# Kernel tuning notes

Hardware: AMD Instinct MI355X
Metric: run time of the kernel (lower is better)

The kernel has to match this reference:

```python
import jax, jax.numpy as jnp
import numpy as np
import itertools
from jax import lax

B, CIN, COUT, RES, NH = 32, 512, 512, 56, 8
STRIDE = RES // 7  # 8 -> post-stride grid is 7x7 (N=49)
HD = COUT // NH    # 64


def _affine(x, s, b):  # BatchNorm2d in inference form (per-channel scale/shift)
    return x * s[None, :, None, None] + b[None, :, None, None]


def _conv1x1(x, w):  # w: [O, C]
    return jnp.einsum('oc,bchw->bohw', w, x)


def _conv3x3(x, w, stride, groups):
    return lax.conv_general_dilated(
        x, w, window_strides=(stride, stride), padding=[(1, 1), (1, 1)],
        feature_group_count=groups, dimension_numbers=('NCHW', 'OIHW', 'NCHW'))


def _bias_idx():
    points = list(itertools.product(range(7), range(7)))
    offsets, idxs = {}, []
    for p1 in points:
        for p2 in points:
            off = (abs(p1[0] - p2[0]), abs(p1[1] - p2[1]))
            if off not in offsets:
                offsets[off] = len(offsets)
            idxs.append(offsets[off])
    return np.array(idxs, dtype=np.int32).reshape(49, 49), len(offsets)


def setup_inputs() -> dict:
    key = jax.random.key(0)
    ks = jax.random.split(key, 24)
    idx_np, n_off = _bias_idx()  # n_off = 49
    rn = lambda k, sh, sc: jax.random.normal(k, sh, dtype=jnp.float32) * sc
    return {
        'x': rn(ks[0], (B, CIN, RES, RES), 1.0),
        'dw_w': rn(ks[1], (CIN, 1, 3, 3), 0.2),
        'bn0_s': 1.0 + rn(ks[2], (CIN,), 0.05), 'bn0_b': rn(ks[3], (CIN,), 0.05),
        'wq': rn(ks[4], (COUT, CIN), 0.03),
        'bnq_s': 1.0 + rn(ks[5], (COUT,), 0.05), 'bnq_b': rn(ks[6], (COUT,), 0.05),
        'wk': rn(ks[7], (COUT, CIN), 0.03),
        'bnk_s': 1.0 + rn(ks[8], (COUT,), 0.05), 'bnk_b': rn(ks[9], (COUT,), 0.05),
        'wv': rn(ks[10], (COUT, CIN), 0.03),
        'bnv_s': 1.0 + rn(ks[11], (COUT,), 0.05), 'bnv_b': rn(ks[12], (COUT,), 0.05),
        'loc_w': rn(ks[13], (COUT, COUT // NH, 3, 3), 0.05), 'loc_b': rn(ks[14], (COUT,), 0.02),
        'bnl_s': 1.0 + rn(ks[15], (COUT,), 0.05), 'bnl_b': rn(ks[16], (COUT,), 0.05),
        'th1': rn(ks[17], (NH, NH), 0.3), 'th2': rn(ks[18], (NH, NH), 0.3),
        'logit_scale': jnp.log(10.0) * jnp.ones((NH, 1, 1), dtype=jnp.float32),
        'ab': rn(ks[19], (NH, n_off), 0.02),
        'wo': rn(ks[20], (COUT, COUT), 0.03),
        'bno_s': 1.0 + rn(ks[21], (COUT,), 0.05), 'bno_b': rn(ks[22], (COUT,), 0.05),
        'bias_idx': jnp.array(idx_np),
    }


def reference(x, dw_w, bn0_s, bn0_b, wq, bnq_s, bnq_b, wk, bnk_s, bnk_b,
              wv, bnv_s, bnv_b, loc_w, loc_b, bnl_s, bnl_b, th1, th2,
              logit_scale, ab, wo, bno_s, bno_b, bias_idx):
    # stride_conv: depthwise 3x3 stride-8 + BN -> [B, C, 7, 7]
    x = _affine(_conv3x3(x, dw_w, STRIDE, CIN), bn0_s, bn0_b)
    Bc, C, H, W = x.shape
    N = H * W  # 49
    q = _affine(_conv1x1(x, wq), bnq_s, bnq_b).reshape(Bc, NH, HD, N).transpose(0, 1, 3, 2)  # [B,H,N,d]
    k = _affine(_conv1x1(x, wk), bnk_s, bnk_b).reshape(Bc, NH, HD, N)                        # [B,H,d,N]
    v4 = _affine(_conv1x1(x, wv), bnv_s, bnv_b)                                              # [B,Cout,7,7]
    v_local = _affine(_conv3x3(v4, loc_w, 1, NH) + loc_b[None, :, None, None], bnl_s, bnl_b)
    v = v4.reshape(Bc, NH, HD, N).transpose(0, 1, 3, 2)                                      # [B,H,N,d]
    # faithful to source: q normalized over head_dim, k normalized over token axis (last)
    qn = q / jnp.maximum(jnp.linalg.norm(q, axis=-1, keepdims=True), 1e-12)
    kn = k / jnp.maximum(jnp.linalg.norm(k, axis=-1, keepdims=True), 1e-12)
    ls = jnp.exp(jnp.minimum(logit_scale, jnp.log(100.0)))  # clamp max then exp
    attn = jnp.einsum('bhnd,bhdm->bhnm', qn, kn) * ls + ab[:, bias_idx]  # [B,H,49,49]
    attn = jnp.einsum('ij,bjnm->binm', th1, attn)   # talking head 1
    attn = jax.nn.softmax(attn, axis=-1)
    attn = jnp.einsum('ij,bjnm->binm', th2, attn)   # talking head 2
    out = jnp.einsum('bhnm,bhmd->bhnd', attn, v)    # [B,H,N,d]
    out = out.transpose(0, 1, 3, 2).reshape(Bc, COUT, H, W) + v_local
    out = jax.image.resize(out, (Bc, COUT, H * STRIDE, W * STRIDE), method='bilinear')
    out = out * jax.nn.relu6(out + 3.0) / 6.0       # Hardswish
    return _affine(_conv1x1(out, wo), bno_s, bno_b)
```

## Files before the change

### kernel.cpp

```cpp
#include <hip/hip_runtime.h>
#include <hip/hip_bf16.h>
#include <stdint.h>

typedef short short8 __attribute__((ext_vector_type(8)));
typedef float f32x4 __attribute__((ext_vector_type(4)));

#define NB    32
#define NC    512
#define NHD   8
#define HDD   64
#define N7    49
#define RES   56
#define P56   3136
#define NTOK  1568
#define NTOKP 1664
#define NBIG  100352
#define KDIM  512
#define KLOC  576

__device__ __forceinline__ void gload_lds16(const __hip_bfloat16* g, __hip_bfloat16* l) {
  __builtin_amdgcn_global_load_lds(
      (const __attribute__((address_space(1))) void*)g,
      (__attribute__((address_space(3))) void*)l, 16, 0, 0);
}

__global__ __launch_bounds__(256) void k_cvt(
    const float* __restrict__ s0, const float* __restrict__ s1,
    const float* __restrict__ s2, const float* __restrict__ s3,
    const float* __restrict__ s4,
    __hip_bfloat16* __restrict__ d0, __hip_bfloat16* __restrict__ d1,
    __hip_bfloat16* __restrict__ d2, __hip_bfloat16* __restrict__ d3,
    __hip_bfloat16* __restrict__ d4) {
  const float* s; __hip_bfloat16* d; int n = NC * NC;
  switch (blockIdx.y) {
    case 0: s = s0; d = d0; break;
    case 1: s = s1; d = d1; break;
    case 2: s = s2; d = d2; break;
    case 3: s = s3; d = d3; break;
    default: s = s4; d = d4; n = NC * KLOC; break;
  }
  for (int i = blockIdx.x * blockDim.x + threadIdx.x; i < n; i += gridDim.x * blockDim.x)
    d[i] = __float2bfloat16(s[i]);
}

__global__ __launch_bounds__(64) void k_stride(
    const float* __restrict__ x, const float* __restrict__ dw,
    const float* __restrict__ s0, const float* __restrict__ b0,
    __hip_bfloat16* __restrict__ xs) {
  const int ci = blockIdx.x, b = blockIdx.y, t = threadIdx.x;
  __shared__ float rows[21][56];
  const float* xp = x + ((size_t)(b * NC + ci)) * RES * RES;
  for (int r = t; r < 21 * 56; r += 64) {
    int rr = r / 56, cc = r - rr * 56;
    int oh = rr / 3, kh = rr - oh * 3;
    int ih = oh * 8 + kh - 1;
    rows[rr][cc] = (ih >= 0) ? xp[ih * 56 + cc] : 0.f;
  }
  float w[9];
#pragma unroll
  for (int j = 0; j < 9; ++j) w[j] = dw[ci * 9 + j];
  const float sc = s0[ci], bi = b0[ci];
  __syncthreads();
  if (t < 49) {
    const int oh = t / 7, ow = t - oh * 7;
    float acc = 0.f;
#pragma unroll
    for (int kh = 0; kh < 3; ++kh)
#pragma unroll
      for (int kw = 0; kw < 3; ++kw) {
        int col = ow * 8 + kw - 1;
        float v = (col >= 0) ? rows[oh * 3 + kh][col] : 0.f;
        acc += v * w[kh * 3 + kw];
      }
    xs[(size_t)(b * 49 + t) * NC + ci] = __float2bfloat16(acc * sc + bi);
  }
}

__global__ __launch_bounds__(512) void k_gemm_big(
    const __hip_bfloat16* __restrict__ A,
    const __hip_bfloat16* __restrict__ Bm,
    const float* __restrict__ scale, const float* __restrict__ bias,
    float* __restrict__ out) {
  __shared__ __align__(16) __hip_bfloat16 lds[2][2][256 * 64];
  const int t = threadIdx.x;
  const int cpx = gridDim.x >> 3;
  const int nid = (blockIdx.x & 7) * cpx + (blockIdx.x >> 3);
  const int m0 = (nid & 1) * 256, n0 = (nid >> 1) * 256;

  const int lane = t & 63, wid = t >> 6;
  const int wm = (wid >> 2) * 128, wn = (wid & 3) * 64;
  const int fr = lane & 15, fq = lane >> 4;
  const int sw = fr & 7;

  const int srow = t >> 3;
  const int scol = ((t & 7) ^ ((t >> 3) & 7)) * 8;
  const __hip_bfloat16* Ab = A  + (size_t)(m0 + srow) * KDIM + scol;
  const __hip_bfloat16* Bb = Bm + (size_t)(n0 + srow) * KDIM + scol;

  const f32x4 fz = {0.f, 0.f, 0.f, 0.f};
  f32x4 acc[8][4];
#pragma unroll
  for (int i = 0; i < 8; ++i)
#pragma unroll
    for (int j = 0; j < 4; ++j) acc[i][j] = fz;

#define STAGE_BIG(d, kt)                                                      \
  do {                                                                        \
    const int kofs = (kt) * 64;                                               \
    gload_lds16(Ab + kofs,              &lds[d][0][wid * 512]);               \
    gload_lds16(Ab + kofs +  64 * KDIM, &lds[d][0][4096  + wid * 512]);       \
    gload_lds16(Ab + kofs + 128 * KDIM, &lds[d][0][8192  + wid * 512]);       \
    gload_lds16(Ab + kofs + 192 * KDIM, &lds[d][0][12288 + wid * 512]);       \
    gload_lds16(Bb + kofs,              &lds[d][1][wid * 512]);               \
    gload_lds16(Bb + kofs +  64 * KDIM, &lds[d][1][4096  + wid * 512]);       \
    gload_lds16(Bb + kofs + 128 * KDIM, &lds[d][1][8192  + wid * 512]);       \
    gload_lds16(Bb + kofs + 192 * KDIM, &lds[d][1][12288 + wid * 512]);       \
  } while (0)

  STAGE_BIG(0, 0);
  STAGE_BIG(1, 1);
  int cur = 0;
#pragma unroll 1
  for (int it = 0; it < 8; ++it) {
    if (it < 7) asm volatile("s_waitcnt vmcnt(8)" ::: "memory");
    else        asm volatile("s_waitcnt vmcnt(0)" ::: "memory");
    __builtin_amdgcn_sched_barrier(0);
    __builtin_amdgcn_s_barrier();
    __builtin_amdgcn_sched_barrier(0);
    const __hip_bfloat16* lap = lds[cur][0];
    const __hip_bfloat16* lbp = lds[cur][1];
#pragma unroll
    for (int ks = 0; ks < 2; ++ks) {
      short8 af[8], bf[4];
      const int c16 = ((ks * 4 + fq) ^ sw) * 8;
#pragma unroll
      for (int mi = 0; mi < 8; ++mi)
        af[mi] = *(const short8*)(lap + (wm + mi * 16 + fr) * 64 + c16);
#pragma unroll
      for (int ni = 0; ni < 4; ++ni)
        bf[ni] = *(const short8*)(lbp + (wn + ni * 16 + fr) * 64 + c16);
      __builtin_amdgcn_s_setprio(1);
#pragma unroll
      for (int mi = 0; mi < 8; ++mi)
#pragma unroll
        for (int ni = 0; ni < 4; ++ni)
          acc[mi][ni] = __builtin_amdgcn_mfma_f32_16x16x32_bf16(af[mi], bf[ni], acc[mi][ni], 0, 0, 0);
      __builtin_amdgcn_s_setprio(0);
    }
    __builtin_amdgcn_sched_barrier(0);
    __builtin_amdgcn_s_barrier();
    __builtin_amdgcn_sched_barrier(0);
    if (it < 6) STAGE_BIG(cur, it + 2);
    cur ^= 1;
  }
#undef STAGE_BIG

#pragma unroll
  for (int mi = 0; mi < 8; ++mi) {
#pragma unroll
    for (int ni = 0; ni < 4; ++ni) {
      const int gn = n0 + wn + ni * 16 + fr;
      const int outer = gn / P56;
      const int ii = gn - outer * P56;
#pragma unroll
      for (int r = 0; r < 4; ++r) {
        const int co = m0 + wm + mi * 16 + fq * 4 + r;
        out[((size_t)outer * NC + co) * P56 + ii] = acc[mi][ni][r] * scale[co] + bias[co];
      }
    }
  }
}

__global__ __launch_bounds__(256) void k_gemm_qkv(
    const __hip_bfloat16* __restrict__ wqb, const __hip_bfloat16* __restrict__ wkb,
    const __hip_bfloat16* __restrict__ wvb, const __hip_bfloat16* __restrict__ xs,
    const float* __restrict__ sq, const float* __restrict__ bq,
    const float* __restrict__ sk, const float* __restrict__ bk,
    const float* __restrict__ sv, const float* __restrict__ bv,
    float* __restrict__ qb, float* __restrict__ kb, float* __restrict__ vb) {
  __shared__ __align__(16) __hip_bfloat16 la[2][128 * 32];
  __shared__ __align__(16) __hip_bfloat16 lb[2][128 * 32];
  const int t = threadIdx.x;
  const int nwg = gridDim.x;
  const int orig = blockIdx.x;
  const int q = nwg >> 3, r = nwg & 7;
  const int xcd = orig & 7, pos = orig >> 3;
  const int nid = (xcd < r ? xcd * (q + 1) : r * (q + 1) + (xcd - r) * q) + pos;
  const int mt = nid % 12, nt = nid / 12;
  const int n0 = nt * 128, m0 = (mt & 3) * 128, sel = mt >> 2;

  const __hip_bfloat16* A = (sel == 0 ? wqb : sel == 1 ? wkb : wvb);
  const float* scale = (sel == 0 ? sq : sel == 1 ? sk : sv);
  const float* bias  = (sel == 0 ? bq : sel == 1 ? bk : bv);
  float* out = (sel == 0 ? qb : sel == 1 ? kb : vb);

  const int lane = t & 63, wid = t >> 6;
  const int wm = (wid >> 1) * 64, wn = (wid & 1) * 64;
  const int fr = lane & 15, fq = lane >> 4, kg = fq * 8;
  const int rA0 = wid * 16;
  const int grow = lane >> 2;
  const int gcol = (lane & 3) * 8;

  const f32x4 fz = {0.f, 0.f, 0.f, 0.f};
  f32x4 acc[4][4];
#pragma unroll
  for (int i = 0; i < 4; ++i)
#pragma unroll
    for (int j = 0; j < 4; ++j) acc[i][j] = fz;

  const __hip_bfloat16* Ab = A + (size_t)(m0 + rA0 + grow) * KDIM + gcol;
  const __hip_bfloat16* Bb = xs + (size_t)(n0 + rA0 + grow) * KDIM + gcol;

#define STAGE_QKV(buf, k0)                                        \
  do {                                                            \
    gload_lds16(Ab + (k0),             la[buf] + rA0 * 32);       \
    gload_lds16(Ab + (k0) + 64 * KDIM, la[buf] + (rA0 + 64) * 32);\
    gload_lds16(Bb + (k0),             lb[buf] + rA0 * 32);       \
    gload_lds16(Bb + (k0) + 64 * KDIM, lb[buf] + (rA0 + 64) * 32);\
  } while (0)

  STAGE_QKV(0, 0);
  STAGE_QKV(1, 32);
  int cur = 0;
#pragma unroll 1
  for (int it = 0; it < 16; ++it) {
    if (it < 15) asm volatile("s_waitcnt vmcnt(4)" ::: "memory");
    else         asm volatile("s_waitcnt vmcnt(0)" ::: "memory");
    __builtin_amdgcn_sched_barrier(0);
    __builtin_amdgcn_s_barrier();
    __builtin_amdgcn_sched_barrier(0);
    const __hip_bfloat16* lap = la[cur];
    const __hip_bfloat16* lbp = lb[cur];
    short8 af[4], bf[4];
#pragma unroll
    for (int mi = 0; mi < 4; ++mi) af[mi] = *(const short8*)(lap + (wm + mi * 16 + fr) * 32 + kg);
#pragma unroll
    for (int ni = 0; ni < 4; ++ni) bf[ni] = *(const short8*)(lbp + (wn + ni * 16 + fr) * 32 + kg);
#pragma unroll
    for (int mi = 0; mi < 4; ++mi)
#pragma unroll
      for (int ni = 0; ni < 4; ++ni)
        acc[mi][ni] = __builtin_amdgcn_mfma_f32_16x16x32_bf16(af[mi], bf[ni], acc[mi][ni], 0, 0, 0);
    __builtin_amdgcn_sched_barrier(0);
    __builtin_amdgcn_s_barrier();
    __builtin_amdgcn_sched_barrier(0);
    if (it < 14) STAGE_QKV(cur, (it + 2) * 32);
    cur ^= 1;
  }
#undef STAGE_QKV

#pragma unroll
  for (int mi = 0; mi < 4; ++mi) {
#pragma unroll
    for (int ni = 0; ni < 4; ++ni) {
      const int gn = n0 + wn + ni * 16 + fr;
      if (gn >= NTOK) continue;
      const int b = gn / 49, ii = gn - b * 49;
#pragma unroll
      for (int r = 0; r < 4; ++r) {
        const int co = m0 + wm + mi * 16 + fq * 4 + r;
        out[((size_t)b * NC + co) * 49 + ii] = acc[mi][ni][r] * scale[co] + bias[co];
      }
    }
  }
}

__global__ __launch_bounds__(256) void k_im2col(
    const float* __restrict__ vb, __hip_bfloat16* __restrict__ bloc) {
  const int g = blockIdx.x, b = blockIdx.y, t = threadIdx.x;
  __shared__ __hip_bfloat16 pad[64][81];
  for (int i = t; i < 64 * 81; i += 256) pad[i / 81][i % 81] = __float2bfloat16(0.f);
  __syncthreads();
  const float* src = vb + ((size_t)b * NC + g * 64) * 49;
  for (int i = t; i < 64 * 49; i += 256) {
    const int ci = i / 49, n = i - ci * 49;
    const int oh = n / 7, ow = n - oh * 7;
    pad[ci][(oh + 1) * 9 + (ow + 1)] = __float2bfloat16(src[i]);
  }
  __syncthreads();
  __hip_bfloat16* dst = bloc + ((size_t)g * NTOK + (size_t)b * 49) * KLOC;
  for (int i = t; i < 49 * KLOC; i += 256) {
    const int n = i / KLOC, k = i - n * KLOC;
    const int ci = k / 9, tap = k - ci * 9;
    const int kh = tap / 3, kw = tap - kh * 3;
    const int oh = n / 7, ow = n - oh * 7;
    dst[i] = pad[ci][(oh + kh) * 9 + (ow + kw)];
  }
}

__global__ __launch_bounds__(256) void k_vloc_gemm(
    const __hip_bfloat16* __restrict__ lwb,
    const __hip_bfloat16* __restrict__ bloc,
    const float* __restrict__ lbias, const float* __restrict__ sl,
    const float* __restrict__ bl, float* __restrict__ vloc) {
  __shared__ __align__(16) unsigned short la[64][40];
  __shared__ __align__(16) unsigned short lb[128][40];
  const int t = threadIdx.x;
  const int g = blockIdx.y;
  const int n0 = blockIdx.x * 128;
  const int lane = t & 63, wid = t >> 6;
  const int wm = (wid >> 1) * 32, wn = (wid & 1) * 64;
  const int fr = lane & 15, fq = lane >> 4, kg = fq * 8;

  const f32x4 fz = {0.f, 0.f, 0.f, 0.f};
  f32x4 acc[2][4];
#pragma unroll
  for (int i = 0; i < 2; ++i)
#pragma unroll
    for (int j = 0; j < 4; ++j) acc[i][j] = fz;

  const int r0 = t >> 2, kk = (t & 3) * 8;
  const short8 z8 = {0, 0, 0, 0, 0, 0, 0, 0};
  const __hip_bfloat16* As = lwb + (size_t)g * 64 * KLOC;
  const __hip_bfloat16* Bs = bloc + (size_t)g * NTOK * KLOC;

  for (int k0 = 0; k0 < KLOC; k0 += 32) {
    __syncthreads();
    *(short8*)(&la[r0][kk]) = *(const short8*)(As + (size_t)r0 * KLOC + k0 + kk);
#pragma unroll
    for (int rr = 0; rr < 128; rr += 64) {
      const int row = r0 + rr;
      const int gn = n0 + row;
      short8 vb8 = z8;
      if (gn < NTOK) vb8 = *(const short8*)(Bs + (size_t)gn * KLOC + k0 + kk);
      *(short8*)(&lb[row][kk]) = vb8;
    }
    __syncthreads();
    short8 af[2], bfv[4];
#pragma unroll
    for (int mi = 0; mi < 2; ++mi) af[mi] = *(const short8*)(&la[wm + mi * 16 + fr][kg]);
#pragma unroll
    for (int ni = 0; ni < 4; ++ni) bfv[ni] = *(const short8*)(&lb[wn + ni * 16 + fr][kg]);
#pragma unroll
    for (int mi = 0; mi < 2; ++mi)
#pragma unroll
      for (int ni = 0; ni < 4; ++ni)
        acc[mi][ni] = __builtin_amdgcn_mfma_f32_16x16x32_bf16(af[mi], bfv[ni], acc[mi][ni], 0, 0, 0);
  }

#pragma unroll
  for (int mi = 0; mi < 2; ++mi) {
#pragma unroll
    for (int ni = 0; ni < 4; ++ni) {
      const int gn = n0 + wn + ni * 16 + fr;
      if (gn >= NTOK) continue;
      const int b = gn / 49, n = gn - b * 49;
#pragma unroll
      for (int r = 0; r < 4; ++r) {
        const int oc = g * 64 + wm + mi * 16 + fq * 4 + r;
        const float sc = sl[oc];
        vloc[((size_t)b * NC + oc) * 49 + n] = acc[mi][ni][r] * sc + lbias[oc] * sc + bl[oc];
      }
    }
  }
}

__global__ __launch_bounds__(256) void k_attn1(
    const float* __restrict__ qb, const float* __restrict__ kb,
    const float* __restrict__ lsc, const float* __restrict__ ab, const int* __restrict__ bidx,
    float* __restrict__ Sbuf) {
  const int h = blockIdx.x, b = blockIdx.y, t = threadIdx.x;
  __shared__ float qt[64 * 49], kt[64 * 49], nq[49], abl[49];
  const float* qs = qb + ((size_t)b * NC + h * 64) * 49;
  const float* ks = kb + ((size_t)b * NC + h * 64) * 49;
  for (int i = t; i < 64 * 49; i += 256) { qt[i] = qs[i]; kt[i] = ks[i]; }
  if (t < 49) abl[t] = ab[h * 49 + t];
  __syncthreads();
  if (t < 49) {
    float s = 0.f;
    for (int d = 0; d < 64; ++d) { float v = qt[d * 49 + t]; s += v * v; }
    nq[t] = fmaxf(sqrtf(s), 1e-12f);
  } else if (t >= 64 && t < 128) {
    const int d = t - 64;
    float s = 0.f;
    for (int m = 0; m < 49; ++m) { float v = kt[d * 49 + m]; s += v * v; }
    const float inv = 1.f / fmaxf(sqrtf(s), 1e-12f);
    for (int m = 0; m < 49; ++m) kt[d * 49 + m] *= inv;
  }
  __syncthreads();
  const float ls = expf(fminf(lsc[h], logf(100.f)));
  for (int idx = t; idx < 49 * 49; idx += 256) {
    const int n = idx / 49, m = idx - n * 49;
    float acc = 0.f;
    for (int d = 0; d < 64; ++d) acc += qt[d * 49 + n] * kt[d * 49 + m];
    Sbuf[(((size_t)b * NHD + h) * 49 + n) * 49 + m] = acc / nq[n] * ls + abl[bidx[idx]];
  }
}

__global__ __launch_bounds__(256) void k_attn2(
    const float* __restrict__ Sbuf, const float* __restrict__ th1, const float* __restrict__ th2,
    const float* __restrict__ vb, const float* __restrict__ vloc, float* __restrict__ y7) {
  const int n = blockIdx.x, b = blockIdx.y, t = threadIdx.x;
  __shared__ float sS[8][49], sP[8][49], sQ[8][49];
  __shared__ float t1[64], t2[64], rsuminv[8];
  if (t < 64) { t1[t] = th1[t]; t2[t] = th2[t]; }
  for (int i = t; i < 392; i += 256) {
    const int j = i / 49, m = i - j * 49;
    sS[j][m] = Sbuf[(((size_t)b * NHD + j) * 49 + n) * 49 + m];
  }
  __syncthreads();
  for (int i = t; i < 392; i += 256) {
    const int j = i / 49, m = i - j * 49;
    float a = 0.f;
#pragma unroll
    for (int jj = 0; jj < 8; ++jj) a += t1[j * 8 + jj] * sS[jj][m];
    sP[j][m] = a;
  }
  __syncthreads();
  if (t < 8) {
    float mx = -1e30f;
    for (int m = 0; m < 49; ++m) mx = fmaxf(mx, sP[t][m]);
    float s = 0.f;
    for (int m = 0; m < 49; ++m) { float e = expf(sP[t][m] - mx); sP[t][m] = e; s += e; }
    rsuminv[t] = 1.f / s;
  }
  __syncthreads();
  for (int i = t; i < 392; i += 256) {
    const int j = i / 49, m = i - j * 49;
    float a = 0.f;
#pragma unroll
    for (int jj = 0; jj < 8; ++jj) a += t2[j * 8 + jj] * (sP[jj][m] * rsuminv[jj]);
    sQ[j][m] = a;
  }
  __syncthreads();
  for (int c = t; c < NC; c += 256) {
    const int hh = c >> 6;
    const float* vp = vb + ((size_t)b * NC + c) * 49;
    float a = 0.f;
    for (int m = 0; m < 49; ++m) a += sQ[hh][m] * vp[m];
    a += vloc[((size_t)b * NC + c) * 49 + n];
    y7[((size_t)b * 49 + n) * NC + c] = a;
  }
}

__global__ __launch_bounds__(256) void k_resize(const float* __restrict__ y7,
                                                __hip_bfloat16* __restrict__ h) {
  const int y = blockIdx.x, b = blockIdx.y, t = threadIdx.x;
  __shared__ float L[2][7][512];
  float sy = (y - 3.5f) * 0.125f;
  sy = fminf(fmaxf(sy, 0.f), 6.f);
  const int iy0 = min((int)floorf(sy), 5);
  const float wy = sy - (float)iy0;
  const float* src = y7 + ((size_t)b * 49 + iy0 * 7) * NC;
  float* Lf = &L[0][0][0];
  for (int i = t; i < 2 * 7 * 512; i += 256) Lf[i] = src[i];
  __syncthreads();
  const size_t outb = ((size_t)b * P56 + (size_t)y * 56) * NC;
  const int c0 = t * 2;
  for (int x = 0; x < 56; ++x) {
    float sx = (x - 3.5f) * 0.125f;
    sx = fminf(fmaxf(sx, 0.f), 6.f);
    const int ix0 = min((int)floorf(sx), 5);
    const float wx = sx - (float)ix0;
    const float w00 = (1.f - wy) * (1.f - wx), w01 = (1.f - wy) * wx;
    const float w10 = wy * (1.f - wx),         w11 = wy * wx;
    float hs[2];
#pragma unroll
    for (int j = 0; j < 2; ++j) {
      const int c = c0 + j;
      const float v = w00 * L[0][ix0][c] + w01 * L[0][ix0 + 1][c]
                    + w10 * L[1][ix0][c] + w11 * L[1][ix0 + 1][c];
      hs[j] = v * fminf(fmaxf(v + 3.f, 0.f), 6.f) * (1.f / 6.f);
    }
    __hip_bfloat162 p;
    p.x = __float2bfloat16(hs[0]);
    p.y = __float2bfloat16(hs[1]);
    *(__hip_bfloat162*)(&h[outb + (size_t)x * NC + c0]) = p;
  }
}

extern "C" void kernel_launch(void* const* d_in, const int* in_sizes, int n_in,
                              void* d_out, int out_size, void* d_ws, size_t ws_size,
                              hipStream_t stream) {
  (void)in_sizes; (void)n_in; (void)out_size; (void)ws_size;
  const float* x     = (const float*)d_in[0];
  const float* dw_w  = (const float*)d_in[1];
  const float* bn0_s = (const float*)d_in[2];
  const float* bn0_b = (const float*)d_in[3];
  const float* wq    = (const float*)d_in[4];
  const float* bnq_s = (const float*)d_in[5];
  const float* bnq_b = (const float*)d_in[6];
  const float* wk    = (const float*)d_in[7];
  const float* bnk_s = (const float*)d_in[8];
  const float* bnk_b = (const float*)d_in[9];
  const float* wv    = (const float*)d_in[10];
  const float* bnv_s = (const float*)d_in[11];
  const float* bnv_b = (const float*)d_in[12];
  const float* loc_w = (const float*)d_in[13];
  const float* loc_b = (const float*)d_in[14];
  const float* bnl_s = (const float*)d_in[15];
  const float* bnl_b = (const float*)d_in[16];
  const float* th1   = (const float*)d_in[17];
  const float* th2   = (const float*)d_in[18];
  const float* lsc   = (const float*)d_in[19];
  const float* ab    = (const float*)d_in[20];
  const float* wo    = (const float*)d_in[21];
  const float* bno_s = (const float*)d_in[22];
  const float* bno_b = (const float*)d_in[23];
  const int*   bidx  = (const int*)d_in[24];

  char* w = (char*)d_ws;
  auto alloc = [&](size_t bytes) {
    char* p = w;
    w += (bytes + 255) & ~(size_t)255;
    return p;
  };
  __hip_bfloat16* h_buf = (__hip_bfloat16*)alloc((size_t)NBIG * NC * 2);
  __hip_bfloat16* wq_b  = (__hip_bfloat16*)alloc((size_t)NC * NC * 2);
  __hip_bfloat16* wk_b  = (__hip_bfloat16*)alloc((size_t)NC * NC * 2);
  __hip_bfloat16* wv_b  = (__hip_bfloat16*)alloc((size_t)NC * NC * 2);
  __hip_bfloat16* wo_b  = (__hip_bfloat16*)alloc((size_t)NC * NC * 2);
  __hip_bfloat16* lw_b  = (__hip_bfloat16*)alloc((size_t)NC * KLOC * 2);
  __hip_bfloat16* xs    = (__hip_bfloat16*)alloc((size_t)NTOKP * NC * 2);
  float* qb   = (float*)alloc((size_t)NB * NC * 49 * 4);
  float* kb   = (float*)alloc((size_t)NB * NC * 49 * 4);
  float* vb   = (float*)alloc((size_t)NB * NC * 49 * 4);
  float* vloc = (float*)alloc((size_t)NB * NC * 49 * 4);
  float* y7   = (float*)alloc((size_t)NB * 49 * NC * 4);
  float* Sb   = (float*)alloc((size_t)NB * NHD * 49 * 49 * 4);
  __hip_bfloat16* bloc = (__hip_bfloat16*)h_buf;

  k_cvt<<<dim3(128, 5), 256, 0, stream>>>(wq, wk, wv, wo, loc_w,
                                          wq_b, wk_b, wv_b, wo_b, lw_b);
  k_stride<<<dim3(NC, NB), 64, 0, stream>>>(x, dw_w, bn0_s, bn0_b, xs);
  k_gemm_qkv<<<dim3(13 * 12), 256, 0, stream>>>(wq_b, wk_b, wv_b, xs,
                                                bnq_s, bnq_b, bnk_s, bnk_b, bnv_s, bnv_b,
                                                qb, kb, vb);
  k_im2col<<<dim3(NHD, NB), 256, 0, stream>>>(vb, bloc);
  k_vloc_gemm<<<dim3(13, NHD), 256, 0, stream>>>(lw_b, bloc, loc_b, bnl_s, bnl_b, vloc);
  k_attn1<<<dim3(NHD, NB), 256, 0, stream>>>(qb, kb, lsc, ab, bidx, Sb);
  k_attn2<<<dim3(49, NB), 256, 0, stream>>>(Sb, th1, th2, vb, vloc, y7);
  k_resize<<<dim3(RES, NB), 256, 0, stream>>>(y7, h_buf);
  k_gemm_big<<<dim3(784), 512, 0, stream>>>(wo_b, h_buf, bno_s, bno_b, (float*)d_out);
}
```

Measured before the change: 267.6 us.

## Restructure big GEMM into 4-stage K=32 pipeline with interleaved quadrant loads

The output-projection GEMM moves from a double-buffered K=64 tile to a four-buffer ring of K=32 tiles for A and B. Each K step is split into four quadrant phases, and each phase issues one slice of the prefetch for tile t+2 while its MFMAs run, with a new XOR swizzle for the narrower rows. The aim is to spread global-to-LDS traffic evenly across the MFMA work and hide load latency better. The cost is many more s_barrier calls per K step and smaller MFMA batches between syncs.

```diff
diff --git a/kernel.cpp b/kernel.cpp
--- a/kernel.cpp
+++ b/kernel.cpp
@@ -81,7 +81,8 @@
     const __hip_bfloat16* __restrict__ Bm,
     const float* __restrict__ scale, const float* __restrict__ bias,
     float* __restrict__ out) {
-  __shared__ __align__(16) __hip_bfloat16 lds[2][2][256 * 64];
+  __shared__ __align__(16) __hip_bfloat16 lsA[4][256 * 32];
+  __shared__ __align__(16) __hip_bfloat16 lsB[4][256 * 32];
   const int t = threadIdx.x;
   const int cpx = gridDim.x >> 3;
   const int nid = (blockIdx.x & 7) * cpx + (blockIdx.x >> 3);
@@ -90,10 +91,10 @@
   const int lane = t & 63, wid = t >> 6;
   const int wm = (wid >> 2) * 128, wn = (wid & 3) * 64;
   const int fr = lane & 15, fq = lane >> 4;
-  const int sw = fr & 7;
-
-  const int srow = t >> 3;
-  const int scol = ((t & 7) ^ ((t >> 3) & 7)) * 8;
+  const int rslot = (fq ^ ((fr >> 1) & 3)) * 8;
+
+  const int srow = t >> 2;
+  const int scol = ((t & 3) ^ ((t >> 3) & 3)) * 8;
   const __hip_bfloat16* Ab = A  + (size_t)(m0 + srow) * KDIM + scol;
   const __hip_bfloat16* Bb = Bm + (size_t)(n0 + srow) * KDIM + scol;
 
@@ -104,56 +105,66 @@
 #pragma unroll
     for (int j = 0; j < 4; ++j) acc[i][j] = fz;
 
-#define STAGE_BIG(d, kt)                                                      \
-  do {                                                                        \
-    const int kofs = (kt) * 64;                                               \
-    gload_lds16(Ab + kofs,              &lds[d][0][wid * 512]);               \
-    gload_lds16(Ab + kofs +  64 * KDIM, &lds[d][0][4096  + wid * 512]);       \
-    gload_lds16(Ab + kofs + 128 * KDIM, &lds[d][0][8192  + wid * 512]);       \
-    gload_lds16(Ab + kofs + 192 * KDIM, &lds[d][0][12288 + wid * 512]);       \
-    gload_lds16(Bb + kofs,              &lds[d][1][wid * 512]);               \
-    gload_lds16(Bb + kofs +  64 * KDIM, &lds[d][1][4096  + wid * 512]);       \
-    gload_lds16(Bb + kofs + 128 * KDIM, &lds[d][1][8192  + wid * 512]);       \
-    gload_lds16(Bb + kofs + 192 * KDIM, &lds[d][1][12288 + wid * 512]);       \
-  } while (0)
-
-  STAGE_BIG(0, 0);
-  STAGE_BIG(1, 1);
-  int cur = 0;
+#define STA(tile, call) gload_lds16(Ab + (tile) * 32 + (size_t)(call) * 128 * KDIM, \
+                                    lsA[(tile) & 3] + (call) * 4096 + wid * 512)
+#define STB(tile, call) gload_lds16(Bb + (tile) * 32 + (size_t)(call) * 128 * KDIM, \
+                                    lsB[(tile) & 3] + (call) * 4096 + wid * 512)
+
+  STA(0, 0); STA(0, 1); STB(0, 0); STB(0, 1);
+  STA(1, 0); STA(1, 1); STB(1, 0); STB(1, 1);
+  asm volatile("s_waitcnt vmcnt(4)" ::: "memory");
+  __builtin_amdgcn_sched_barrier(0);
+  __builtin_amdgcn_s_barrier();
+  __builtin_amdgcn_sched_barrier(0);
+
 #pragma unroll 1
-  for (int it = 0; it < 8; ++it) {
-    if (it < 7) asm volatile("s_waitcnt vmcnt(8)" ::: "memory");
-    else        asm volatile("s_waitcnt vmcnt(0)" ::: "memory");
-    __builtin_amdgcn_sched_barrier(0);
-    __builtin_amdgcn_s_barrier();
-    __builtin_amdgcn_sched_barrier(0);
-    const __hip_bfloat16* lap = lds[cur][0];
-    const __hip_bfloat16* lbp = lds[cur][1];
-#pragma unroll
-    for (int ks = 0; ks < 2; ++ks) {
-      short8 af[8], bf[4];
-      const int c16 = ((ks * 4 + fq) ^ sw) * 8;
-#pragma unroll
-      for (int mi = 0; mi < 8; ++mi)
-        af[mi] = *(const short8*)(lap + (wm + mi * 16 + fr) * 64 + c16);
-#pragma unroll
-      for (int ni = 0; ni < 4; ++ni)
-        bf[ni] = *(const short8*)(lbp + (wn + ni * 16 + fr) * 64 + c16);
+  for (int tt = 0; tt < 16; ++tt) {
+    const __hip_bfloat16* lA = lsA[tt & 3];
+    const __hip_bfloat16* lB = lsB[tt & 3];
+    const int ft = tt + 2;
+#pragma unroll
+    for (int q = 0; q < 4; ++q) {
+      short8 af[4], bf[2];
+#pragma unroll
+      for (int i = 0; i < 4; ++i)
+        af[i] = *(const short8*)(lA + (wm + (q >> 1) * 64 + i * 16 + fr) * 32 + rslot);
+#pragma unroll
+      for (int i = 0; i < 2; ++i)
+        bf[i] = *(const short8*)(lB + (wn + (q & 1) * 32 + i * 16 + fr) * 32 + rslot);
+      if (ft < 16) {
+        if (q == 0)      STA(ft, 0);
+        else if (q == 1) STA(ft, 1);
+        else if (q == 2) STB(ft, 0);
+        else             STB(ft, 1);
+      }
+      __builtin_amdgcn_sched_barrier(0);
+      __builtin_amdgcn_s_barrier();
+      asm volatile("s_waitcnt lgkmcnt(0)" ::: "memory");
+      __builtin_amdgcn_sched_barrier(0);
       __builtin_amdgcn_s_setprio(1);
 #pragma unroll
-      for (int mi = 0; mi < 8; ++mi)
-#pragma unroll
-        for (int ni = 0; ni < 4; ++ni)
-          acc[mi][ni] = __builtin_amdgcn_mfma_f32_16x16x32_bf16(af[mi], bf[ni], acc[mi][ni], 0, 0, 0);
+      for (int i = 0; i < 4; ++i)
+#pragma unroll
+        for (int j = 0; j < 2; ++j)
+          acc[(q >> 1) * 4 + i][(q & 1) * 2 + j] = __builtin_amdgcn_mfma_f32_16x16x32_bf16(
+              af[i], bf[j], acc[(q >> 1) * 4 + i][(q & 1) * 2 + j], 0, 0, 0);
       __builtin_amdgcn_s_setprio(0);
-    }
-    __builtin_amdgcn_sched_barrier(0);
-    __builtin_amdgcn_s_barrier();
-    __builtin_amdgcn_sched_barrier(0);
-    if (it < 6) STAGE_BIG(cur, it + 2);
-    cur ^= 1;
-  }
-#undef STAGE_BIG
+      __builtin_amdgcn_sched_barrier(0);
+      if (q < 3) {
+        __builtin_amdgcn_s_barrier();
+        __builtin_amdgcn_sched_barrier(0);
+      }
+    }
+    if (tt < 15) {
+      if (tt < 14) asm volatile("s_waitcnt vmcnt(4)" ::: "memory");
+      else         asm volatile("s_waitcnt vmcnt(0)" ::: "memory");
+      __builtin_amdgcn_sched_barrier(0);
+      __builtin_amdgcn_s_barrier();
+      __builtin_amdgcn_sched_barrier(0);
+    }
+  }
+#undef STA
+#undef STB
 
 #pragma unroll
   for (int mi = 0; mi < 8; ++mi) {
```

New measurement: 292.4 us. 9.3% more time.
